# Kernel optimization log

Hardware: AMD Instinct MI355X
Metric: run time of the kernel (lower is better)

## Reference

```python
import jax, jax.numpy as jnp
import numpy as np

N, E, D = 50000, 600000, 128


def setup_inputs() -> dict:
    key = jax.random.key(0)
    ks = jax.random.split(key, 16)
    s = 0.05
    inp = {
        "x": jax.random.normal(ks[0], (N, D), dtype=jnp.float32),
        "Wv": jax.random.normal(ks[1], (D, D), dtype=jnp.float32) * s,
        "bv": jnp.zeros((D,), dtype=jnp.float32),
        "Wa": jax.random.normal(ks[2], (D, D), dtype=jnp.float32) * s,
        "ba": jnp.zeros((D,), dtype=jnp.float32),
        "Wm1": jax.random.normal(ks[3], (D, D), dtype=jnp.float32) * s,
        "bm1": jnp.zeros((D,), dtype=jnp.float32),
        "Wm2": jax.random.normal(ks[4], (D, D), dtype=jnp.float32) * s,
        "bm2": jnp.zeros((D,), dtype=jnp.float32),
        "Wp1": jax.random.normal(ks[5], (D, D), dtype=jnp.float32) * s,
        "bp1": jnp.zeros((D,), dtype=jnp.float32),
        "Wp2": jax.random.normal(ks[6], (D, D), dtype=jnp.float32) * s,
        "bp2": jnp.zeros((D,), dtype=jnp.float32),
        "edge_index": jax.random.randint(ks[7], (2, E), 0, N, dtype=jnp.int64),
        "batch": jnp.zeros((N,), dtype=jnp.int64),
        "passes": 4,
    }
    return inp


def reference(x, Wv, bv, Wa, ba, Wm1, bm1, Wm2, bm2, Wp1, bp1, Wp2, bp2,
              edge_index, batch, passes):
    src, dst = edge_index[0], edge_index[1]
    n = x.shape[0]
    h = x
    for _ in range(passes):
        # gather source features, sum-aggregate at destination nodes
        aggr = jax.ops.segment_sum(h[src], dst, num_segments=n)  # [N, D]
        # update: V(h) + min(h, A(aggr)); V/A are Linear+ReLU (1-layer MLP)
        upd = jax.nn.relu(h @ Wv + bv) + jnp.minimum(h, jax.nn.relu(aggr @ Wa + ba))
        # combine MLP (2 layers: Linear-ReLU-Linear)
        upd = jax.nn.relu(upd @ Wm1 + bm1) @ Wm2 + bm2
        h = jax.nn.relu(upd)
    # final prediction: two stacked Linears, no activation between
    return (h @ Wp1 + bp1) @ Wp2 + bp2
```

## Files before the change

kernel.cpp:

```cpp
#include <hip/hip_runtime.h>

#define D 128

typedef _Float16 half8 __attribute__((ext_vector_type(8)));
typedef float f32x4 __attribute__((ext_vector_type(4)));

__device__ __forceinline__ float frelu(float x) { return fmaxf(x, 0.f); }

__global__ void count_kernel(const int* __restrict__ dst, int E, int* __restrict__ deg) {
    int e = blockIdx.x * blockDim.x + threadIdx.x;
    if (e < E) atomicAdd(&deg[dst[e]], 1);
}

__global__ void scan_kernel(const int* __restrict__ deg, int* __restrict__ rowstart, int n) {
    const int T = 1024;
    __shared__ int part[T];
    int tid = threadIdx.x;
    int chunk = (n + T - 1) / T;
    int beg = tid * chunk;
    int end = min(beg + chunk, n);
    int s = 0;
    for (int i = beg; i < end; ++i) s += deg[i];
    part[tid] = s;
    __syncthreads();
    for (int off = 1; off < T; off <<= 1) {
        int v = 0;
        if (tid >= off) v = part[tid - off];
        __syncthreads();
        if (tid >= off) part[tid] += v;
        __syncthreads();
    }
    int prefix = (tid == 0) ? 0 : part[tid - 1];
    for (int i = beg; i < end; ++i) {
        rowstart[i] = prefix;
        prefix += deg[i];
    }
    if (tid == T - 1) rowstart[n] = prefix;
}

__global__ void fill_kernel(const int* __restrict__ src, const int* __restrict__ dst, int E,
                            const int* __restrict__ rowstart, int* __restrict__ cursor,
                            int* __restrict__ bucket) {
    int e = blockIdx.x * blockDim.x + threadIdx.x;
    if (e < E) {
        int d = dst[e];
        int pos = atomicAdd(&cursor[d], 1);
        bucket[rowstart[d] + pos] = src[e];
    }
}

__global__ void gather_kernel(const float* __restrict__ h, const int* __restrict__ rowstart,
                              const int* __restrict__ bucket, float* __restrict__ aggr, int n) {
    int node = blockIdx.x * 4 + (threadIdx.x >> 6);
    if (node >= n) return;
    int lane = threadIdx.x & 63;
    const float2* __restrict__ h2 = reinterpret_cast<const float2*>(h);
    int s = rowstart[node], e = rowstart[node + 1];
    float2 a[8];
#pragma unroll
    for (int m = 0; m < 8; ++m) a[m] = float2{0.f, 0.f};
    int j = s;
    for (; j + 8 <= e; j += 8) {
#pragma unroll
        for (int m = 0; m < 8; ++m) {
            float2 v = h2[(size_t)bucket[j + m] * 64 + lane];
            a[m].x += v.x; a[m].y += v.y;
        }
    }
    for (; j < e; ++j) {
        float2 v = h2[(size_t)bucket[j] * 64 + lane];
        a[0].x += v.x; a[0].y += v.y;
    }
    float2 r;
    r.x = ((a[0].x + a[1].x) + (a[2].x + a[3].x)) + ((a[4].x + a[5].x) + (a[6].x + a[7].x));
    r.y = ((a[0].y + a[1].y) + (a[2].y + a[3].y)) + ((a[4].y + a[5].y) + (a[6].y + a[7].y));
    reinterpret_cast<float2*>(aggr)[(size_t)node * 64 + lane] = r;
}

__global__ void pack_kernel(const float* __restrict__ W0, const float* __restrict__ W1,
                            const float* __restrict__ W2, const float* __restrict__ W3,
                            const float* __restrict__ W4, const float* __restrict__ W5,
                            _Float16* __restrict__ pk) {
    const float* Ws[6] = {W0, W1, W2, W3, W4, W5};
    const float* __restrict__ W = Ws[blockIdx.x];
    half8* __restrict__ base = reinterpret_cast<half8*>(pk) + (size_t)blockIdx.x * 4096;
    for (int it = threadIdx.x; it < 2048; it += 256) {
        int lane = it & 63, ks = (it >> 6) & 3, cf = it >> 8;
        int c = cf * 16 + (lane & 15);
        half8 hv, lv;
#pragma unroll
        for (int e = 0; e < 8; ++e) {
            int k = ks * 32 + ((e < 4) ? 0 : 16) + (lane >> 4) * 4 + (e & 3);
            float w = W[k * 128 + c];
            _Float16 hi = (_Float16)w;
            hv[e] = hi;
            lv[e] = (_Float16)(w - (float)hi);
        }
        base[(cf * 4 + ks) * 64 + lane] = hv;
        base[2048 + (cf * 4 + ks) * 64 + lane] = lv;
    }
}


__device__ __forceinline__ void split8(const float4 x0, const float4 x1, half8& hh, half8& ll) {
    float xs[8] = {x0.x, x0.y, x0.z, x0.w, x1.x, x1.y, x1.z, x1.w};
#pragma unroll
    for (int e = 0; e < 8; ++e) {
        _Float16 hi = (_Float16)xs[e];
        hh[e] = hi;
        ll[e] = (_Float16)(xs[e] - (float)hi);
    }
}

enum { M_P1, M_P2, M_RELU_BAND, M_RELU_GLOB, M_BIAS_BAND, M_BIAS_GLOB };

template <int MODE, bool A_GLOBAL>
__device__ __forceinline__ void phase(const float4* __restrict__ Ag,
                                      float4* __restrict__ B4,
                                      float* __restrict__ sB,
                                      const half8* __restrict__ pkm,
                                      const float* __restrict__ bias,
                                      const float* __restrict__ hsrc,
                                      float* __restrict__ gout,
                                      int lane, int band0, int n) {
    const int lr = lane & 15;
    const int kb = lane >> 4;
    const int cl = lane & 15;
    const int lrb = (lane >> 4) * 4;

    half8 ah[4], al[4];
    if constexpr (A_GLOBAL) {
        const float4 z = {0.f, 0.f, 0.f, 0.f};
        const int row = band0 + lr;
        const float4* __restrict__ base = Ag + (size_t)row * 32;
        const bool ok = row < n;
#pragma unroll
        for (int ks = 0; ks < 4; ++ks) {
            float4 x0 = ok ? base[ks * 8 + kb] : z;
            float4 x1 = ok ? base[ks * 8 + 4 + kb] : z;
            split8(x0, x1, ah[ks], al[ks]);
        }
    } else {
        const int key = lr & 7;
#pragma unroll
        for (int ks = 0; ks < 4; ++ks) {
            float4 x0 = B4[lr * 32 + ((ks * 8 + kb) ^ key)];
            float4 x1 = B4[lr * 32 + ((ks * 8 + 4 + kb) ^ key)];
            split8(x0, x1, ah[ks], al[ks]);
        }
    }

    float bb[8];
#pragma unroll
    for (int cf = 0; cf < 8; ++cf) bb[cf] = bias[cf * 16 + cl];

    const half8* __restrict__ ph = pkm;
    const half8* __restrict__ pl = pkm + 2048;

    half8 bh[2][4], bl[2][4];
#pragma unroll
    for (int ks = 0; ks < 4; ++ks) {
        bh[0][ks] = ph[ks * 64 + lane];
        bl[0][ks] = pl[ks * 64 + lane];
    }

#pragma unroll
    for (int cf = 0; cf < 8; ++cf) {
        const int cur = cf & 1, nxt = cur ^ 1;
        if (cf < 7) {
#pragma unroll
            for (int ks = 0; ks < 4; ++ks) {
                bh[nxt][ks] = ph[((cf + 1) * 4 + ks) * 64 + lane];
                bl[nxt][ks] = pl[((cf + 1) * 4 + ks) * 64 + lane];
            }
        }
        f32x4 a = {0.f, 0.f, 0.f, 0.f};
#pragma unroll
        for (int ks = 0; ks < 4; ++ks) {
            a = __builtin_amdgcn_mfma_f32_16x16x32_f16(ah[ks], bh[cur][ks], a, 0, 0, 0);
            a = __builtin_amdgcn_mfma_f32_16x16x32_f16(al[ks], bh[cur][ks], a, 0, 0, 0);
            a = __builtin_amdgcn_mfma_f32_16x16x32_f16(ah[ks], bl[cur][ks], a, 0, 0, 0);
            a = __builtin_amdgcn_mfma_f32_16x16x32_f16(al[ks], bl[cur][ks], a, 0, 0, 0);
        }
        const int c = cf * 16 + cl;
        const int cq = c >> 2, cr = c & 3;
#pragma unroll
        for (int g = 0; g < 4; ++g) {
            const int r = lrb + g;
            const int slot = cq ^ (r & 7);
            float* __restrict__ addr = &sB[r * 128 + slot * 4 + cr];
            float v = a[g] + bb[cf];
            if constexpr (MODE == M_P1) {
                *addr = frelu(v);
            } else if constexpr (MODE == M_P2) {
                float u1 = *addr;
                int gr = band0 + r;
                float hv = (gr < n) ? hsrc[(size_t)gr * D + c] : 0.f;
                *addr = frelu(v) + fminf(hv, u1);
            } else if constexpr (MODE == M_RELU_BAND) {
                *addr = frelu(v);
            } else if constexpr (MODE == M_BIAS_BAND) {
                *addr = v;
            } else if constexpr (MODE == M_RELU_GLOB) {
                int gr = band0 + r;
                if (gr < n) gout[(size_t)gr * D + c] = frelu(v);
            } else {
                int gr = band0 + r;
                if (gr < n) gout[(size_t)gr * D + c] = v;
            }
        }
    }
}

__launch_bounds__(64)
__global__ void update_kernel(const float* __restrict__ h, const float* __restrict__ aggr,
                              const _Float16* __restrict__ pk,
                              const float* __restrict__ bv, const float* __restrict__ ba,
                              const float* __restrict__ bm1, const float* __restrict__ bm2,
                              float* __restrict__ hout, int n) {
    __shared__ float4 B4[512];
    float* sB = reinterpret_cast<float*>(B4);
    const int lane = threadIdx.x;
    const int band0 = blockIdx.x * 16;
    const half8* __restrict__ pk8 = reinterpret_cast<const half8*>(pk);
    const float4* __restrict__ h4 = reinterpret_cast<const float4*>(h);
    const float4* __restrict__ a4 = reinterpret_cast<const float4*>(aggr);

    phase<M_P1, true>(a4, B4, sB, pk8 + 0 * 4096, ba, nullptr, nullptr, lane, band0, n);
    phase<M_P2, true>(h4, B4, sB, pk8 + 1 * 4096, bv, h, nullptr, lane, band0, n);
    phase<M_RELU_BAND, false>(nullptr, B4, sB, pk8 + 2 * 4096, bm1, nullptr, nullptr, lane, band0, n);
    phase<M_RELU_GLOB, false>(nullptr, B4, sB, pk8 + 3 * 4096, bm2, nullptr, hout, lane, band0, n);
}

__launch_bounds__(64)
__global__ void final_kernel(const float* __restrict__ h, const _Float16* __restrict__ pk,
                             const float* __restrict__ bp1, const float* __restrict__ bp2,
                             float* __restrict__ out, int n) {
    __shared__ float4 B4[512];
    float* sB = reinterpret_cast<float*>(B4);
    const int lane = threadIdx.x;
    const int band0 = blockIdx.x * 16;
    const half8* __restrict__ pk8 = reinterpret_cast<const half8*>(pk);
    const float4* __restrict__ h4 = reinterpret_cast<const float4*>(h);

    phase<M_BIAS_BAND, true>(h4, B4, sB, pk8 + 4 * 4096, bp1, nullptr, nullptr, lane, band0, n);
    phase<M_BIAS_GLOB, false>(nullptr, B4, sB, pk8 + 5 * 4096, bp2, nullptr, out, lane, band0, n);
}

extern "C" void kernel_launch(void* const* d_in, const int* in_sizes, int n_in,
                              void* d_out, int out_size, void* d_ws, size_t ws_size,
                              hipStream_t stream) {
    const float* x   = (const float*)d_in[0];
    const float* Wv  = (const float*)d_in[1];
    const float* bv  = (const float*)d_in[2];
    const float* Wa  = (const float*)d_in[3];
    const float* ba  = (const float*)d_in[4];
    const float* Wm1 = (const float*)d_in[5];
    const float* bm1 = (const float*)d_in[6];
    const float* Wm2 = (const float*)d_in[7];
    const float* bm2 = (const float*)d_in[8];
    const float* Wp1 = (const float*)d_in[9];
    const float* bp1 = (const float*)d_in[10];
    const float* Wp2 = (const float*)d_in[11];
    const float* bp2 = (const float*)d_in[12];
    const int* ei    = (const int*)d_in[13];

    const int N = in_sizes[0] / D;
    const int E = in_sizes[13] / 2;
    const int* src = ei;
    const int* dst = ei + E;

    char* ws = (char*)d_ws;
    size_t off = 0;
    auto alloc = [&](size_t bytes) -> void* {
        void* p = ws + off;
        off += (bytes + 255) & ~(size_t)255;
        return p;
    };
    float* hb0  = (float*)alloc((size_t)N * D * sizeof(float));
    float* hb1  = (float*)alloc((size_t)N * D * sizeof(float));
    float* aggr = (float*)alloc((size_t)N * D * sizeof(float));
    int* deg      = (int*)alloc((size_t)(N + 1) * sizeof(int));
    int* rowstart = (int*)alloc((size_t)(N + 1) * sizeof(int));
    int* cursor   = (int*)alloc((size_t)(N + 1) * sizeof(int));
    int* bucket   = (int*)alloc((size_t)E * sizeof(int));
    _Float16* pk  = (_Float16*)alloc((size_t)6 * 2 * 128 * 128 * sizeof(_Float16));

    hipMemsetAsync(deg, 0, (size_t)(N + 1) * sizeof(int), stream);
    hipMemsetAsync(cursor, 0, (size_t)(N + 1) * sizeof(int), stream);

    pack_kernel<<<6, 256, 0, stream>>>(Wa, Wv, Wm1, Wm2, Wp1, Wp2, pk);

    int eb = (E + 255) / 256;
    count_kernel<<<eb, 256, 0, stream>>>(dst, E, deg);
    scan_kernel<<<1, 1024, 0, stream>>>(deg, rowstart, N);
    fill_kernel<<<eb, 256, 0, stream>>>(src, dst, E, rowstart, cursor, bucket);

    int ub = (N + 15) / 16;
    int gb = (N + 3) / 4;
    const float* cur = x;
    float* bufs[2] = {hb0, hb1};
    for (int p = 0; p < 4; ++p) {
        gather_kernel<<<gb, 256, 0, stream>>>(cur, rowstart, bucket, aggr, N);
        float* nxt = bufs[p & 1];
        update_kernel<<<ub, 64, 0, stream>>>(cur, aggr, pk, bv, ba, bm1, bm2, nxt, N);
        cur = nxt;
    }
    final_kernel<<<ub, 64, 0, stream>>>(cur, pk, bp1, bp2, (float*)d_out, N);
}
```

Before: 623.7 us.

## Parallelize CSR prefix scan and widen gather loads to float4 with half-wave split

Replaces the single-block serial-chunk scan with a three-stage multi-block scan: block reductions, a scan of the block sums, then per-block expansion. This removes a latency-bound one-block kernel. The gather kernel now uses float4 loads, with each half-wavefront processing alternate neighbor edges, and combines the halves with a cross-lane shuffle. This halves the load instruction count and doubles the edges in flight. The block-sum scan assumes at most 256 blocks, which holds for N=50000 (196 blocks) but is not general.

```diff
diff --git a/kernel.cpp b/kernel.cpp
--- a/kernel.cpp
+++ b/kernel.cpp
@@ -12,30 +12,55 @@
     if (e < E) atomicAdd(&deg[dst[e]], 1);
 }
 
-__global__ void scan_kernel(const int* __restrict__ deg, int* __restrict__ rowstart, int n) {
-    const int T = 1024;
-    __shared__ int part[T];
-    int tid = threadIdx.x;
-    int chunk = (n + T - 1) / T;
-    int beg = tid * chunk;
-    int end = min(beg + chunk, n);
-    int s = 0;
-    for (int i = beg; i < end; ++i) s += deg[i];
-    part[tid] = s;
+__global__ void scan_partial(const int* __restrict__ deg, int* __restrict__ bsum, int n) {
+    __shared__ int red[256];
+    int i = blockIdx.x * 256 + threadIdx.x;
+    red[threadIdx.x] = (i < n) ? deg[i] : 0;
     __syncthreads();
-    for (int off = 1; off < T; off <<= 1) {
-        int v = 0;
-        if (tid >= off) v = part[tid - off];
-        __syncthreads();
-        if (tid >= off) part[tid] += v;
-        __syncthreads();
-    }
-    int prefix = (tid == 0) ? 0 : part[tid - 1];
-    for (int i = beg; i < end; ++i) {
-        rowstart[i] = prefix;
-        prefix += deg[i];
-    }
-    if (tid == T - 1) rowstart[n] = prefix;
+#pragma unroll
+    for (int off = 128; off > 0; off >>= 1) {
+        if (threadIdx.x < off) red[threadIdx.x] += red[threadIdx.x + off];
+        __syncthreads();
+    }
+    if (threadIdx.x == 0) bsum[blockIdx.x] = red[0];
+}
+
+__global__ void scan_bsum(const int* __restrict__ bsum, int* __restrict__ bpre,
+                          int* __restrict__ rowstart, int nb, int n) {
+    __shared__ int s[256];
+    int t = threadIdx.x;
+    int v = (t < nb) ? bsum[t] : 0;
+    s[t] = v;
+    __syncthreads();
+#pragma unroll
+    for (int off = 1; off < 256; off <<= 1) {
+        int u = 0;
+        if (t >= off) u = s[t - off];
+        __syncthreads();
+        if (t >= off) s[t] += u;
+        __syncthreads();
+    }
+    if (t < nb) bpre[t] = s[t] - v;
+    if (t == 255) rowstart[n] = s[255];
+}
+
+__global__ void scan_expand(const int* __restrict__ deg, const int* __restrict__ bpre,
+                            int* __restrict__ rowstart, int n) {
+    __shared__ int s[256];
+    int b = blockIdx.x, t = threadIdx.x;
+    int i = b * 256 + t;
+    int v = (i < n) ? deg[i] : 0;
+    s[t] = v;
+    __syncthreads();
+#pragma unroll
+    for (int off = 1; off < 256; off <<= 1) {
+        int u = 0;
+        if (t >= off) u = s[t - off];
+        __syncthreads();
+        if (t >= off) s[t] += u;
+        __syncthreads();
+    }
+    if (i < n) rowstart[i] = bpre[b] + s[t] - v;
 }
 
 __global__ void fill_kernel(const int* __restrict__ src, const int* __restrict__ dst, int E,
@@ -54,27 +79,39 @@
     int node = blockIdx.x * 4 + (threadIdx.x >> 6);
     if (node >= n) return;
     int lane = threadIdx.x & 63;
-    const float2* __restrict__ h2 = reinterpret_cast<const float2*>(h);
+    int col = lane & 31, hf = lane >> 5;
+    const float4* __restrict__ h4 = reinterpret_cast<const float4*>(h);
     int s = rowstart[node], e = rowstart[node + 1];
-    float2 a[8];
-#pragma unroll
-    for (int m = 0; m < 8; ++m) a[m] = float2{0.f, 0.f};
+    float4 a[8];
+#pragma unroll
+    for (int m = 0; m < 8; ++m) a[m] = float4{0.f, 0.f, 0.f, 0.f};
     int j = s;
-    for (; j + 8 <= e; j += 8) {
+    for (; j + 16 <= e; j += 16) {
 #pragma unroll
         for (int m = 0; m < 8; ++m) {
-            float2 v = h2[(size_t)bucket[j + m] * 64 + lane];
-            a[m].x += v.x; a[m].y += v.y;
-        }
-    }
-    for (; j < e; ++j) {
-        float2 v = h2[(size_t)bucket[j] * 64 + lane];
-        a[0].x += v.x; a[0].y += v.y;
-    }
-    float2 r;
+            float4 v = h4[(size_t)bucket[j + 2 * m + hf] * 32 + col];
+            a[m].x += v.x; a[m].y += v.y; a[m].z += v.z; a[m].w += v.w;
+        }
+    }
+    for (; j + 2 <= e; j += 2) {
+        float4 v = h4[(size_t)bucket[j + hf] * 32 + col];
+        a[0].x += v.x; a[0].y += v.y; a[0].z += v.z; a[0].w += v.w;
+    }
+    if (j < e && hf == 0) {
+        float4 v = h4[(size_t)bucket[j] * 32 + col];
+        a[0].x += v.x; a[0].y += v.y; a[0].z += v.z; a[0].w += v.w;
+    }
+    float4 r;
     r.x = ((a[0].x + a[1].x) + (a[2].x + a[3].x)) + ((a[4].x + a[5].x) + (a[6].x + a[7].x));
     r.y = ((a[0].y + a[1].y) + (a[2].y + a[3].y)) + ((a[4].y + a[5].y) + (a[6].y + a[7].y));
-    reinterpret_cast<float2*>(aggr)[(size_t)node * 64 + lane] = r;
+    r.z = ((a[0].z + a[1].z) + (a[2].z + a[3].z)) + ((a[4].z + a[5].z) + (a[6].z + a[7].z));
+    r.w = ((a[0].w + a[1].w) + (a[2].w + a[3].w)) + ((a[4].w + a[5].w) + (a[6].w + a[7].w));
+    r.x += __shfl(r.x, lane ^ 32);
+    r.y += __shfl(r.y, lane ^ 32);
+    r.z += __shfl(r.z, lane ^ 32);
+    r.w += __shfl(r.w, lane ^ 32);
+    if (hf == 0)
+        reinterpret_cast<float4*>(aggr)[(size_t)node * 32 + col] = r;
 }
 
 __global__ void pack_kernel(const float* __restrict__ W0, const float* __restrict__ W1,
@@ -284,6 +321,8 @@
     int* rowstart = (int*)alloc((size_t)(N + 1) * sizeof(int));
     int* cursor   = (int*)alloc((size_t)(N + 1) * sizeof(int));
     int* bucket   = (int*)alloc((size_t)E * sizeof(int));
+    int* bsum     = (int*)alloc(256 * sizeof(int));
+    int* bpre     = (int*)alloc(256 * sizeof(int));
     _Float16* pk  = (_Float16*)alloc((size_t)6 * 2 * 128 * 128 * sizeof(_Float16));
 
     hipMemsetAsync(deg, 0, (size_t)(N + 1) * sizeof(int), stream);
@@ -292,8 +331,11 @@
     pack_kernel<<<6, 256, 0, stream>>>(Wa, Wv, Wm1, Wm2, Wp1, Wp2, pk);
 
     int eb = (E + 255) / 256;
+    int nb = (N + 255) / 256;
     count_kernel<<<eb, 256, 0, stream>>>(dst, E, deg);
-    scan_kernel<<<1, 1024, 0, stream>>>(deg, rowstart, N);
+    scan_partial<<<nb, 256, 0, stream>>>(deg, bsum, N);
+    scan_bsum<<<1, 256, 0, stream>>>(bsum, bpre, rowstart, nb, N);
+    scan_expand<<<nb, 256, 0, stream>>>(deg, bpre, rowstart, N);
     fill_kernel<<<eb, 256, 0, stream>>>(src, dst, E, rowstart, cursor, bucket);
 
     int ub = (N + 15) / 16;
```

New measurement: 560.5 us. 10.1% less time.
